# Kernel optimization log

Measured on AMD Instinct MI355X. Metric: run time of the kernel, lower is better.

Reference implementation:

```python
import jax, jax.numpy as jnp
import numpy as np

NNZ = 1_000_000
M = N = 8192
K = 128

def setup_inputs() -> dict:
    key = jax.random.key(0)
    k1, k2, k3, k4, k5 = jax.random.split(key, 5)
    mask_vals = jax.random.normal(k1, (NNZ,), dtype=jnp.float32)
    rows = jax.random.randint(k2, (NNZ,), 0, M, dtype=jnp.int64)
    cols = jax.random.randint(k3, (NNZ,), 0, N, dtype=jnp.int64)
    mat1 = jax.random.normal(k4, (M, K), dtype=jnp.float32)
    mat2 = jax.random.normal(k5, (K, N), dtype=jnp.float32)
    return {"mask_vals": mask_vals, "rows": rows, "cols": cols,
            "mat1": mat1, "mat2": mat2}

def reference(mask_vals, rows, cols, mat1, mat2):
    # torch.sparse.sampled_addmm with alpha=beta=1:
    # out.values = mask.values + (mat1 @ mat2)[rows, cols]
    # SDDMM: only compute the dot products at the sampled (row, col) pairs.
    a = mat1[rows]        # [nnz, K] gather of mat1 rows
    b = mat2[:, cols].T   # [nnz, K] gather of mat2 cols
    sampled = jnp.einsum('nk,nk->n', a, b)  # per-nnz dot product
    return mask_vals + sampled
```

## Files before the change

### kernel.cpp

```cpp
#include <hip/hip_runtime.h>
#include <hip/hip_fp16.h>


#define KDIM 128
#define NBUCK 64
#define SLAB_COLS 128
#define NBLK 512
#define SUBS 16

typedef _Float16 half2v __attribute__((ext_vector_type(2)));

union F4H8 {
  float4 f4;
  half2v h2[4];
  _Float16 h[8];
};


__global__ __launch_bounds__(256) void convert_f16_kernel(
    const float* __restrict__ in, _Float16* __restrict__ out, int n) {
  int i = (blockIdx.x * 256 + threadIdx.x) * 8;
  if (i >= n) return;
  const float4* p = (const float4*)(in + i);
  float4 x0 = p[0];
  float4 x1 = p[1];
  F4H8 o;
  o.h[0] = (_Float16)x0.x; o.h[1] = (_Float16)x0.y;
  o.h[2] = (_Float16)x0.z; o.h[3] = (_Float16)x0.w;
  o.h[4] = (_Float16)x1.x; o.h[5] = (_Float16)x1.y;
  o.h[6] = (_Float16)x1.z; o.h[7] = (_Float16)x1.w;
  *(float4*)(out + i) = o.f4;
}

__global__ __launch_bounds__(256) void transpose_f16_kernel(
    const float* __restrict__ in, _Float16* __restrict__ out, int N) {
  __shared__ float tile[32][33];
  int bx = blockIdx.x * 32;
  int by = blockIdx.y * 32;
  int tx = threadIdx.x;
  int ty = threadIdx.y;
#pragma unroll
  for (int j = 0; j < 32; j += 8) {
    tile[ty + j][tx] = in[(size_t)(by + ty + j) * N + (bx + tx)];
  }
  __syncthreads();
#pragma unroll
  for (int j = 0; j < 32; j += 8) {
    out[(size_t)(bx + ty + j) * KDIM + (by + tx)] = (_Float16)tile[tx][ty + j];
  }
}


__global__ __launch_bounds__(256) void hist_kernel(
    const int* __restrict__ cols, int nnz, int epb,
    int* __restrict__ blockHist) {
  __shared__ int h[NBUCK];
  if (threadIdx.x < NBUCK) h[threadIdx.x] = 0;
  __syncthreads();
  int lo = blockIdx.x * epb;
  int hi = min(lo + epb, nnz);
  for (int i = lo + threadIdx.x; i < hi; i += 256) {
    atomicAdd(&h[cols[i] >> 7], 1);
  }
  __syncthreads();
  if (threadIdx.x < NBUCK) {
    blockHist[blockIdx.x * NBUCK + threadIdx.x] = h[threadIdx.x];
  }
}

__global__ __launch_bounds__(NBLK) void colscan_kernel(
    const int* __restrict__ blockHist, int* __restrict__ blockScan,
    int* __restrict__ totals) {
  __shared__ int sh[NBLK];
  int b = blockIdx.x;
  int t = threadIdx.x;
  int v = blockHist[t * NBUCK + b];
  sh[t] = v;
  __syncthreads();
  for (int off = 1; off < NBLK; off <<= 1) {
    int x = (t >= off) ? sh[t - off] : 0;
    __syncthreads();
    sh[t] += x;
    __syncthreads();
  }
  blockScan[t * NBUCK + b] = sh[t] - v;
  if (t == NBLK - 1) totals[b] = sh[t];
}

__global__ __launch_bounds__(64) void base_kernel(
    const int* __restrict__ totals, int* __restrict__ bucketBase) {
  if (threadIdx.x == 0) {
    int acc = 0;
    for (int b = 0; b < NBUCK; ++b) {
      bucketBase[b] = acc;
      acc += totals[b];
      acc = (acc + 7) & ~7;
    }
    bucketBase[NBUCK] = acc;
  }
}

__global__ __launch_bounds__(256) void scatter_kernel(
    const int* __restrict__ rows, const int* __restrict__ cols,
    const float* __restrict__ mask, int nnz, int epb,
    const int* __restrict__ blockScan, const int* __restrict__ bucketBase,
    int* __restrict__ sortedRC, float* __restrict__ sortedMask,
    int* __restrict__ sortedIdx) {
  __shared__ int h[NBUCK];
  if (threadIdx.x < NBUCK) h[threadIdx.x] = 0;
  __syncthreads();
  int blk = blockIdx.x;
  int lo = blk * epb;
  int hi = min(lo + epb, nnz);
  for (int i = lo + threadIdx.x; i < hi; i += 256) {
    int c = cols[i];
    int r = rows[i];
    float mv = mask[i];
    int b = c >> 7;
    int rank = atomicAdd(&h[b], 1);
    int pos = bucketBase[b] + blockScan[blk * NBUCK + b] + rank;
    sortedRC[pos] = (r << 16) | c;
    sortedMask[pos] = mv;
    sortedIdx[pos] = i;
  }
}


__device__ __forceinline__ float dot8(const F4H8& a, const F4H8& b) {
  float s = 0.f;
#if __has_builtin(__builtin_amdgcn_fdot2)
#pragma unroll
  for (int j = 0; j < 4; ++j) s = __builtin_amdgcn_fdot2(a.h2[j], b.h2[j], s, false);
#else
#pragma unroll
  for (int j = 0; j < 8; ++j) s += (float)a.h[j] * (float)b.h[j];
#endif
  return s;
}

__device__ __forceinline__ float red16(float s) {
  s += __shfl_xor(s, 8);
  s += __shfl_xor(s, 4);
  s += __shfl_xor(s, 2);
  s += __shfl_xor(s, 1);
  return s;
}

__global__ __launch_bounds__(512) void sddmm_slab_kernel(
    const _Float16* __restrict__ m1,
    const _Float16* __restrict__ m2t,
    const int* __restrict__ sortedRC,
    const float* __restrict__ sortedMask,
    const int* __restrict__ sortedIdx,
    const int* __restrict__ bucketBase,
    const int* __restrict__ totals,
    float* __restrict__ out) {
  __shared__ _Float16 slab[SLAB_COLS * KDIM];
  int s = blockIdx.x / SUBS;
  int sub = blockIdx.x % SUBS;

  {
    const float4* src = (const float4*)(m2t + (size_t)s * SLAB_COLS * KDIM);
    float4* dst = (float4*)slab;
#pragma unroll
    for (int i = 0; i < (SLAB_COLS * KDIM / 8) / 512; ++i) {
      dst[threadIdx.x + i * 512] = src[threadIdx.x + i * 512];
    }
  }
  __syncthreads();

  int start = bucketBase[s];
  int cnt = totals[s];
  int hi0 = start + cnt;
  int per = ((cnt + SUBS - 1) / SUBS + 3) & ~3;
  int lo = start + sub * per;
  int hi = min(lo + per, hi0);

  int grp = threadIdx.x >> 4;
  int lane = threadIdx.x & 15;

  for (int g0 = lo + grp * 4; g0 < hi; g0 += 32 * 4) {
    if (g0 + 4 <= hi) {
      int4 rc4 = *(const int4*)(sortedRC + g0);
      float4 mv4 = *(const float4*)(sortedMask + g0);
      int4 idx4 = *(const int4*)(sortedIdx + g0);

      F4H8 a0, a1, a2, a3, b0, b1, b2, b3;
      a0.f4 = ((const float4*)(m1 + (size_t)(rc4.x >> 16) * KDIM))[lane];
      a1.f4 = ((const float4*)(m1 + (size_t)(rc4.y >> 16) * KDIM))[lane];
      a2.f4 = ((const float4*)(m1 + (size_t)(rc4.z >> 16) * KDIM))[lane];
      a3.f4 = ((const float4*)(m1 + (size_t)(rc4.w >> 16) * KDIM))[lane];
      b0.f4 = ((const float4*)(slab + (rc4.x & (SLAB_COLS - 1)) * KDIM))[lane];
      b1.f4 = ((const float4*)(slab + (rc4.y & (SLAB_COLS - 1)) * KDIM))[lane];
      b2.f4 = ((const float4*)(slab + (rc4.z & (SLAB_COLS - 1)) * KDIM))[lane];
      b3.f4 = ((const float4*)(slab + (rc4.w & (SLAB_COLS - 1)) * KDIM))[lane];

      float s0 = red16(dot8(a0, b0));
      float s1 = red16(dot8(a1, b1));
      float s2 = red16(dot8(a2, b2));
      float s3 = red16(dot8(a3, b3));

      if (lane == 0) {
        out[idx4.x] = mv4.x + s0;
        out[idx4.y] = mv4.y + s1;
        out[idx4.z] = mv4.z + s2;
        out[idx4.w] = mv4.w + s3;
      }
    } else {
      for (int g = g0; g < hi; ++g) {
        int rc = sortedRC[g];
        F4H8 a, b;
        a.f4 = ((const float4*)(m1 + (size_t)(rc >> 16) * KDIM))[lane];
        b.f4 = ((const float4*)(slab + (rc & (SLAB_COLS - 1)) * KDIM))[lane];
        float sv = red16(dot8(a, b));
        if (lane == 0) out[sortedIdx[g]] = sortedMask[g] + sv;
      }
    }
  }
}


__global__ __launch_bounds__(256) void sddmm_f16_b4_kernel(
    const float* __restrict__ mask_vals, const int* __restrict__ rows,
    const int* __restrict__ cols, const _Float16* __restrict__ m1,
    const _Float16* __restrict__ m2t, float* __restrict__ out, int nnz) {
  int tid = blockIdx.x * 256 + threadIdx.x;
  int grp = tid >> 4;
  int lane = tid & 15;
  int g0 = grp * 4;
  if (g0 >= nnz) return;
  if (g0 + 4 <= nnz) {
    int4 r4 = *(const int4*)(rows + g0);
    int4 c4 = *(const int4*)(cols + g0);
    F4H8 a0, a1, a2, a3, b0, b1, b2, b3;
    a0.f4 = ((const float4*)(m1 + (size_t)r4.x * KDIM))[lane];
    a1.f4 = ((const float4*)(m1 + (size_t)r4.y * KDIM))[lane];
    a2.f4 = ((const float4*)(m1 + (size_t)r4.z * KDIM))[lane];
    a3.f4 = ((const float4*)(m1 + (size_t)r4.w * KDIM))[lane];
    b0.f4 = ((const float4*)(m2t + (size_t)c4.x * KDIM))[lane];
    b1.f4 = ((const float4*)(m2t + (size_t)c4.y * KDIM))[lane];
    b2.f4 = ((const float4*)(m2t + (size_t)c4.z * KDIM))[lane];
    b3.f4 = ((const float4*)(m2t + (size_t)c4.w * KDIM))[lane];
    float s0 = red16(dot8(a0, b0));
    float s1 = red16(dot8(a1, b1));
    float s2 = red16(dot8(a2, b2));
    float s3 = red16(dot8(a3, b3));
    if (lane == 0) {
      float4 mv = *(const float4*)(mask_vals + g0);
      float4 o = {mv.x + s0, mv.y + s1, mv.z + s2, mv.w + s3};
      *(float4*)(out + g0) = o;
    }
  } else {
    for (int g = g0; g < nnz; ++g) {
      F4H8 a, b;
      a.f4 = ((const float4*)(m1 + (size_t)rows[g] * KDIM))[lane];
      b.f4 = ((const float4*)(m2t + (size_t)cols[g] * KDIM))[lane];
      float sv = red16(dot8(a, b));
      if (lane == 0) out[g] = mask_vals[g] + sv;
    }
  }
}

__global__ __launch_bounds__(256) void sddmm16_strided_kernel(
    const float* __restrict__ mask_vals, const int* __restrict__ rows,
    const int* __restrict__ cols, const float* __restrict__ mat1,
    const float* __restrict__ mat2, float* __restrict__ out, int nnz, int N) {
  int tid = blockIdx.x * 256 + threadIdx.x;
  int g = tid >> 4;
  int lane = tid & 15;
  if (g >= nnz) return;
  int r = rows[g];
  int c = cols[g];
  const float* arow = mat1 + (size_t)r * KDIM;
  float s = 0.f;
#pragma unroll
  for (int j = 0; j < 8; ++j) {
    int k = lane + 16 * j;
    s += arow[k] * mat2[(size_t)k * N + c];
  }
  s = red16(s);
  if (lane == 0) out[g] = mask_vals[g] + s;
}


extern "C" void kernel_launch(void* const* d_in, const int* in_sizes, int n_in,
                              void* d_out, int out_size, void* d_ws, size_t ws_size,
                              hipStream_t stream) {
  const float* mask_vals = (const float*)d_in[0];
  const int*   rows      = (const int*)d_in[1];
  const int*   cols      = (const int*)d_in[2];
  const float* mat1      = (const float*)d_in[3];
  const float* mat2      = (const float*)d_in[4];
  float*       out       = (float*)d_out;

  int nnz   = in_sizes[0];
  int m1_sz = in_sizes[3];
  int N     = in_sizes[4] / KDIM;

  auto align256 = [](size_t x) { return (x + 255) & ~(size_t)255; };
  size_t off = 0;
  size_t o_m1h   = off; off = align256(off + (size_t)m1_sz * 2);
  size_t o_m2th  = off; off = align256(off + (size_t)KDIM * N * 2);
  size_t cap     = (size_t)nnz + 8 * NBUCK + 64;
  size_t o_rc    = off; off = align256(off + cap * 4);
  size_t o_mk    = off; off = align256(off + cap * 4);
  size_t o_ix    = off; off = align256(off + cap * 4);
  size_t o_bh    = off; off = align256(off + (size_t)NBLK * NBUCK * 4);
  size_t o_bs    = off; off = align256(off + (size_t)NBLK * NBUCK * 4);
  size_t o_tot   = off; off = align256(off + NBUCK * 4);
  size_t o_base  = off; off = align256(off + (NBUCK + 1) * 4);
  size_t need_full = off;
  size_t need_min  = align256((size_t)m1_sz * 2) + align256((size_t)KDIM * N * 2);

  char* ws = (char*)d_ws;

  if (ws_size >= need_full && N == 8192) {
    _Float16* m1h   = (_Float16*)(ws + o_m1h);
    _Float16* m2th  = (_Float16*)(ws + o_m2th);
    int*      sRC   = (int*)(ws + o_rc);
    float*    sMK   = (float*)(ws + o_mk);
    int*      sIX   = (int*)(ws + o_ix);
    int*      bh    = (int*)(ws + o_bh);
    int*      bs    = (int*)(ws + o_bs);
    int*      tot   = (int*)(ws + o_tot);
    int*      bbase = (int*)(ws + o_base);

    convert_f16_kernel<<<(m1_sz / 8 + 255) / 256, 256, 0, stream>>>(mat1, m1h, m1_sz);
    dim3 tb(32, 8);
    dim3 tg(N / 32, KDIM / 32);
    transpose_f16_kernel<<<tg, tb, 0, stream>>>(mat2, m2th, N);

    int epb = (nnz + NBLK - 1) / NBLK;
    hist_kernel<<<NBLK, 256, 0, stream>>>(cols, nnz, epb, bh);
    colscan_kernel<<<NBUCK, NBLK, 0, stream>>>(bh, bs, tot);
    base_kernel<<<1, 64, 0, stream>>>(tot, bbase);
    scatter_kernel<<<NBLK, 256, 0, stream>>>(rows, cols, mask_vals, nnz, epb,
                                             bs, bbase, sRC, sMK, sIX);
    sddmm_slab_kernel<<<NBUCK * SUBS, 512, 0, stream>>>(m1h, m2th, sRC, sMK,
                                                        sIX, bbase, tot, out);
  } else if (ws_size >= need_min) {
    _Float16* m1h  = (_Float16*)ws;
    _Float16* m2th = m1h + m1_sz;
    convert_f16_kernel<<<(m1_sz / 8 + 255) / 256, 256, 0, stream>>>(mat1, m1h, m1_sz);
    dim3 tb(32, 8);
    dim3 tg(N / 32, KDIM / 32);
    transpose_f16_kernel<<<tg, tb, 0, stream>>>(mat2, m2th, N);
    int groups = (nnz + 3) / 4;
    int blocks = (groups * 16 + 255) / 256;
    sddmm_f16_b4_kernel<<<blocks, 256, 0, stream>>>(mask_vals, rows, cols, m1h,
                                                    m2th, out, nnz);
  } else {
    int blocks = ((size_t)nnz * 16 + 255) / 256;
    sddmm16_strided_kernel<<<blocks, 256, 0, stream>>>(mask_vals, rows, cols,
                                                       mat1, mat2, out, nnz, N);
  }
}
```

Baseline: 122.6 us.

## Fuse prep kernels, replace block scan with atomic cursors, pack sort records

Merges the fp16 conversion and the transpose into one launch. The per-block histogram and column scan are replaced by global atomic totals, a single-wave shuffle scan, and per-block atomic cursor reservation inside scatter, which now counts locally a second time. Row/col, index and mask are packed into one int4 record per element, so the SDDMM kernel issues one load per element instead of three separate arrays. This cuts the launch count and the scan overhead but makes the bucket ordering nondeterministic, re-reads cols in scatter, and writes 16 bytes per record instead of 12.

```diff
diff --git a/kernel.cpp b/kernel.cpp
--- a/kernel.cpp
+++ b/kernel.cpp
@@ -15,6 +15,208 @@
   half2v h2[4];
   _Float16 h[8];
 };
+
+
+__global__ __launch_bounds__(256) void prep_kernel(
+    const float* __restrict__ mat1, _Float16* __restrict__ m1h, int m1_sz,
+    const float* __restrict__ mat2, _Float16* __restrict__ m2th, int N,
+    int* __restrict__ tot, int nconvblk) {
+  __shared__ float tile[32][33];
+  int blk = blockIdx.x;
+  if (blk < nconvblk) {
+    if (blk == 0 && threadIdx.x < NBUCK) tot[threadIdx.x] = 0;
+    int i = (blk * 256 + threadIdx.x) * 8;
+    if (i < m1_sz) {
+      const float4* p = (const float4*)(mat1 + i);
+      float4 x0 = p[0];
+      float4 x1 = p[1];
+      F4H8 o;
+      o.h[0] = (_Float16)x0.x; o.h[1] = (_Float16)x0.y;
+      o.h[2] = (_Float16)x0.z; o.h[3] = (_Float16)x0.w;
+      o.h[4] = (_Float16)x1.x; o.h[5] = (_Float16)x1.y;
+      o.h[6] = (_Float16)x1.z; o.h[7] = (_Float16)x1.w;
+      *(float4*)(m1h + i) = o.f4;
+    }
+    return;
+  }
+  int u = blk - nconvblk;
+  int nbx = N / 32;
+  int bx = (u % nbx) * 32;
+  int by = (u / nbx) * 32;
+  int tx = threadIdx.x & 31;
+  int ty = threadIdx.x >> 5;
+#pragma unroll
+  for (int j = 0; j < 32; j += 8) {
+    tile[ty + j][tx] = mat2[(size_t)(by + ty + j) * N + (bx + tx)];
+  }
+  __syncthreads();
+#pragma unroll
+  for (int j = 0; j < 32; j += 8) {
+    m2th[(size_t)(bx + ty + j) * KDIM + (by + tx)] = (_Float16)tile[tx][ty + j];
+  }
+}
+
+
+__global__ __launch_bounds__(256) void hist_kernel(
+    const int* __restrict__ cols, int nnz, int epb, int* __restrict__ tot) {
+  __shared__ int h[NBUCK];
+  if (threadIdx.x < NBUCK) h[threadIdx.x] = 0;
+  __syncthreads();
+  int lo = blockIdx.x * epb;
+  int hi = min(lo + epb, nnz);
+  for (int i = lo + threadIdx.x; i < hi; i += 256) {
+    atomicAdd(&h[cols[i] >> 7], 1);
+  }
+  __syncthreads();
+  if (threadIdx.x < NBUCK && h[threadIdx.x]) {
+    atomicAdd(&tot[threadIdx.x], h[threadIdx.x]);
+  }
+}
+
+
+__global__ __launch_bounds__(64) void scan_kernel(
+    const int* __restrict__ tot, int* __restrict__ bbase,
+    int* __restrict__ cursor) {
+  int t = threadIdx.x;
+  int v = (tot[t] + 7) & ~7;
+  int inc = v;
+#pragma unroll
+  for (int off = 1; off < 64; off <<= 1) {
+    int x = __shfl_up(inc, off);
+    if (t >= off) inc += x;
+  }
+  int base = inc - v;
+  bbase[t] = base;
+  cursor[t] = base;
+}
+
+
+__global__ __launch_bounds__(256) void scatter_kernel(
+    const int* __restrict__ rows, const int* __restrict__ cols,
+    const float* __restrict__ mask, int nnz, int epb,
+    int* __restrict__ cursor, int4* __restrict__ recs) {
+  __shared__ int h[NBUCK];
+  __shared__ int startS[NBUCK];
+  if (threadIdx.x < NBUCK) h[threadIdx.x] = 0;
+  __syncthreads();
+  int lo = blockIdx.x * epb;
+  int hi = min(lo + epb, nnz);
+  for (int i = lo + threadIdx.x; i < hi; i += 256) {
+    atomicAdd(&h[cols[i] >> 7], 1);
+  }
+  __syncthreads();
+  if (threadIdx.x < NBUCK) {
+    int c = h[threadIdx.x];
+    startS[threadIdx.x] = c ? atomicAdd(&cursor[threadIdx.x], c) : 0;
+    h[threadIdx.x] = 0;
+  }
+  __syncthreads();
+  for (int i = lo + threadIdx.x; i < hi; i += 256) {
+    int c = cols[i];
+    int b = c >> 7;
+    int rank = atomicAdd(&h[b], 1);
+    int pos = startS[b] + rank;
+    int4 rec;
+    rec.x = (rows[i] << 16) | c;
+    rec.y = i;
+    rec.z = __float_as_int(mask[i]);
+    rec.w = 0;
+    recs[pos] = rec;
+  }
+}
+
+
+__device__ __forceinline__ float dot8(const F4H8& a, const F4H8& b) {
+  float s = 0.f;
+#if __has_builtin(__builtin_amdgcn_fdot2)
+#pragma unroll
+  for (int j = 0; j < 4; ++j) s = __builtin_amdgcn_fdot2(a.h2[j], b.h2[j], s, false);
+#else
+#pragma unroll
+  for (int j = 0; j < 8; ++j) s += (float)a.h[j] * (float)b.h[j];
+#endif
+  return s;
+}
+
+__device__ __forceinline__ float red16(float s) {
+  s += __shfl_xor(s, 8);
+  s += __shfl_xor(s, 4);
+  s += __shfl_xor(s, 2);
+  s += __shfl_xor(s, 1);
+  return s;
+}
+
+__global__ __launch_bounds__(512) void sddmm_slab_kernel(
+    const _Float16* __restrict__ m1,
+    const _Float16* __restrict__ m2t,
+    const int4* __restrict__ recs,
+    const int* __restrict__ bbase,
+    const int* __restrict__ tot,
+    float* __restrict__ out) {
+  __shared__ _Float16 slab[SLAB_COLS * KDIM];
+  int s = blockIdx.x / SUBS;
+  int sub = blockIdx.x % SUBS;
+
+  {
+    const float4* src = (const float4*)(m2t + (size_t)s * SLAB_COLS * KDIM);
+    float4* dst = (float4*)slab;
+#pragma unroll
+    for (int i = 0; i < 4; ++i) {
+      dst[threadIdx.x + i * 512] = src[threadIdx.x + i * 512];
+    }
+  }
+  __syncthreads();
+
+  int start = bbase[s];
+  int cnt = tot[s];
+  int hi0 = start + cnt;
+  int per = ((cnt + SUBS - 1) / SUBS + 3) & ~3;
+  int lo = start + sub * per;
+  int hi = min(lo + per, hi0);
+
+  int grp = threadIdx.x >> 4;
+  int lane = threadIdx.x & 15;
+
+  for (int g0 = lo + grp * 4; g0 < hi; g0 += 32 * 4) {
+    if (g0 + 4 <= hi) {
+      int4 r0 = recs[g0];
+      int4 r1 = recs[g0 + 1];
+      int4 r2 = recs[g0 + 2];
+      int4 r3 = recs[g0 + 3];
+
+      F4H8 a0, a1, a2, a3, b0, b1, b2, b3;
+      a0.f4 = ((const float4*)(m1 + (size_t)((unsigned)r0.x >> 16) * KDIM))[lane];
+      a1.f4 = ((const float4*)(m1 + (size_t)((unsigned)r1.x >> 16) * KDIM))[lane];
+      a2.f4 = ((const float4*)(m1 + (size_t)((unsigned)r2.x >> 16) * KDIM))[lane];
+      a3.f4 = ((const float4*)(m1 + (size_t)((unsigned)r3.x >> 16) * KDIM))[lane];
+      b0.f4 = ((const float4*)(slab + (r0.x & (SLAB_COLS - 1)) * KDIM))[lane];
+      b1.f4 = ((const float4*)(slab + (r1.x & (SLAB_COLS - 1)) * KDIM))[lane];
+      b2.f4 = ((const float4*)(slab + (r2.x & (SLAB_COLS - 1)) * KDIM))[lane];
+      b3.f4 = ((const float4*)(slab + (r3.x & (SLAB_COLS - 1)) * KDIM))[lane];
+
+      float s0 = red16(dot8(a0, b0));
+      float s1 = red16(dot8(a1, b1));
+      float s2 = red16(dot8(a2, b2));
+      float s3 = red16(dot8(a3, b3));
+
+      if (lane == 0) {
+        out[r0.y] = __int_as_float(r0.z) + s0;
+        out[r1.y] = __int_as_float(r1.z) + s1;
+        out[r2.y] = __int_as_float(r2.z) + s2;
+        out[r3.y] = __int_as_float(r3.z) + s3;
+      }
+    } else {
+      for (int g = g0; g < hi; ++g) {
+        int4 r = recs[g];
+        F4H8 a, b;
+        a.f4 = ((const float4*)(m1 + (size_t)((unsigned)r.x >> 16) * KDIM))[lane];
+        b.f4 = ((const float4*)(slab + (r.x & (SLAB_COLS - 1)) * KDIM))[lane];
+        float sv = red16(dot8(a, b));
+        if (lane == 0) out[r.y] = __int_as_float(r.z) + sv;
+      }
+    }
+  }
+}
 
 
 __global__ __launch_bounds__(256) void convert_f16_kernel(
@@ -49,176 +251,6 @@
     out[(size_t)(bx + ty + j) * KDIM + (by + tx)] = (_Float16)tile[tx][ty + j];
   }
 }
-
-
-__global__ __launch_bounds__(256) void hist_kernel(
-    const int* __restrict__ cols, int nnz, int epb,
-    int* __restrict__ blockHist) {
-  __shared__ int h[NBUCK];
-  if (threadIdx.x < NBUCK) h[threadIdx.x] = 0;
-  __syncthreads();
-  int lo = blockIdx.x * epb;
-  int hi = min(lo + epb, nnz);
-  for (int i = lo + threadIdx.x; i < hi; i += 256) {
-    atomicAdd(&h[cols[i] >> 7], 1);
-  }
-  __syncthreads();
-  if (threadIdx.x < NBUCK) {
-    blockHist[blockIdx.x * NBUCK + threadIdx.x] = h[threadIdx.x];
-  }
-}
-
-__global__ __launch_bounds__(NBLK) void colscan_kernel(
-    const int* __restrict__ blockHist, int* __restrict__ blockScan,
-    int* __restrict__ totals) {
-  __shared__ int sh[NBLK];
-  int b = blockIdx.x;
-  int t = threadIdx.x;
-  int v = blockHist[t * NBUCK + b];
-  sh[t] = v;
-  __syncthreads();
-  for (int off = 1; off < NBLK; off <<= 1) {
-    int x = (t >= off) ? sh[t - off] : 0;
-    __syncthreads();
-    sh[t] += x;
-    __syncthreads();
-  }
-  blockScan[t * NBUCK + b] = sh[t] - v;
-  if (t == NBLK - 1) totals[b] = sh[t];
-}
-
-__global__ __launch_bounds__(64) void base_kernel(
-    const int* __restrict__ totals, int* __restrict__ bucketBase) {
-  if (threadIdx.x == 0) {
-    int acc = 0;
-    for (int b = 0; b < NBUCK; ++b) {
-      bucketBase[b] = acc;
-      acc += totals[b];
-      acc = (acc + 7) & ~7;
-    }
-    bucketBase[NBUCK] = acc;
-  }
-}
-
-__global__ __launch_bounds__(256) void scatter_kernel(
-    const int* __restrict__ rows, const int* __restrict__ cols,
-    const float* __restrict__ mask, int nnz, int epb,
-    const int* __restrict__ blockScan, const int* __restrict__ bucketBase,
-    int* __restrict__ sortedRC, float* __restrict__ sortedMask,
-    int* __restrict__ sortedIdx) {
-  __shared__ int h[NBUCK];
-  if (threadIdx.x < NBUCK) h[threadIdx.x] = 0;
-  __syncthreads();
-  int blk = blockIdx.x;
-  int lo = blk * epb;
-  int hi = min(lo + epb, nnz);
-  for (int i = lo + threadIdx.x; i < hi; i += 256) {
-    int c = cols[i];
-    int r = rows[i];
-    float mv = mask[i];
-    int b = c >> 7;
-    int rank = atomicAdd(&h[b], 1);
-    int pos = bucketBase[b] + blockScan[blk * NBUCK + b] + rank;
-    sortedRC[pos] = (r << 16) | c;
-    sortedMask[pos] = mv;
-    sortedIdx[pos] = i;
-  }
-}
-
-
-__device__ __forceinline__ float dot8(const F4H8& a, const F4H8& b) {
-  float s = 0.f;
-#if __has_builtin(__builtin_amdgcn_fdot2)
-#pragma unroll
-  for (int j = 0; j < 4; ++j) s = __builtin_amdgcn_fdot2(a.h2[j], b.h2[j], s, false);
-#else
-#pragma unroll
-  for (int j = 0; j < 8; ++j) s += (float)a.h[j] * (float)b.h[j];
-#endif
-  return s;
-}
-
-__device__ __forceinline__ float red16(float s) {
-  s += __shfl_xor(s, 8);
-  s += __shfl_xor(s, 4);
-  s += __shfl_xor(s, 2);
-  s += __shfl_xor(s, 1);
-  return s;
-}
-
-__global__ __launch_bounds__(512) void sddmm_slab_kernel(
-    const _Float16* __restrict__ m1,
-    const _Float16* __restrict__ m2t,
-    const int* __restrict__ sortedRC,
-    const float* __restrict__ sortedMask,
-    const int* __restrict__ sortedIdx,
-    const int* __restrict__ bucketBase,
-    const int* __restrict__ totals,
-    float* __restrict__ out) {
-  __shared__ _Float16 slab[SLAB_COLS * KDIM];
-  int s = blockIdx.x / SUBS;
-  int sub = blockIdx.x % SUBS;
-
-  {
-    const float4* src = (const float4*)(m2t + (size_t)s * SLAB_COLS * KDIM);
-    float4* dst = (float4*)slab;
-#pragma unroll
-    for (int i = 0; i < (SLAB_COLS * KDIM / 8) / 512; ++i) {
-      dst[threadIdx.x + i * 512] = src[threadIdx.x + i * 512];
-    }
-  }
-  __syncthreads();
-
-  int start = bucketBase[s];
-  int cnt = totals[s];
-  int hi0 = start + cnt;
-  int per = ((cnt + SUBS - 1) / SUBS + 3) & ~3;
-  int lo = start + sub * per;
-  int hi = min(lo + per, hi0);
-
-  int grp = threadIdx.x >> 4;
-  int lane = threadIdx.x & 15;
-
-  for (int g0 = lo + grp * 4; g0 < hi; g0 += 32 * 4) {
-    if (g0 + 4 <= hi) {
-      int4 rc4 = *(const int4*)(sortedRC + g0);
-      float4 mv4 = *(const float4*)(sortedMask + g0);
-      int4 idx4 = *(const int4*)(sortedIdx + g0);
-
-      F4H8 a0, a1, a2, a3, b0, b1, b2, b3;
-      a0.f4 = ((const float4*)(m1 + (size_t)(rc4.x >> 16) * KDIM))[lane];
-      a1.f4 = ((const float4*)(m1 + (size_t)(rc4.y >> 16) * KDIM))[lane];
-      a2.f4 = ((const float4*)(m1 + (size_t)(rc4.z >> 16) * KDIM))[lane];
-      a3.f4 = ((const float4*)(m1 + (size_t)(rc4.w >> 16) * KDIM))[lane];
-      b0.f4 = ((const float4*)(slab + (rc4.x & (SLAB_COLS - 1)) * KDIM))[lane];
-      b1.f4 = ((const float4*)(slab + (rc4.y & (SLAB_COLS - 1)) * KDIM))[lane];
-      b2.f4 = ((const float4*)(slab + (rc4.z & (SLAB_COLS - 1)) * KDIM))[lane];
-      b3.f4 = ((const float4*)(slab + (rc4.w & (SLAB_COLS - 1)) * KDIM))[lane];
-
-      float s0 = red16(dot8(a0, b0));
-      float s1 = red16(dot8(a1, b1));
-      float s2 = red16(dot8(a2, b2));
-      float s3 = red16(dot8(a3, b3));
-
-      if (lane == 0) {
-        out[idx4.x] = mv4.x + s0;
-        out[idx4.y] = mv4.y + s1;
-        out[idx4.z] = mv4.z + s2;
-        out[idx4.w] = mv4.w + s3;
-      }
-    } else {
-      for (int g = g0; g < hi; ++g) {
-        int rc = sortedRC[g];
-        F4H8 a, b;
-        a.f4 = ((const float4*)(m1 + (size_t)(rc >> 16) * KDIM))[lane];
-        b.f4 = ((const float4*)(slab + (rc & (SLAB_COLS - 1)) * KDIM))[lane];
-        float sv = red16(dot8(a, b));
-        if (lane == 0) out[sortedIdx[g]] = sortedMask[g] + sv;
-      }
-    }
-  }
-}
-
 
 __global__ __launch_bounds__(256) void sddmm_f16_b4_kernel(
     const float* __restrict__ mask_vals, const int* __restrict__ rows,
@@ -299,45 +331,38 @@
 
   auto align256 = [](size_t x) { return (x + 255) & ~(size_t)255; };
   size_t off = 0;
-  size_t o_m1h   = off; off = align256(off + (size_t)m1_sz * 2);
-  size_t o_m2th  = off; off = align256(off + (size_t)KDIM * N * 2);
-  size_t cap     = (size_t)nnz + 8 * NBUCK + 64;
-  size_t o_rc    = off; off = align256(off + cap * 4);
-  size_t o_mk    = off; off = align256(off + cap * 4);
-  size_t o_ix    = off; off = align256(off + cap * 4);
-  size_t o_bh    = off; off = align256(off + (size_t)NBLK * NBUCK * 4);
-  size_t o_bs    = off; off = align256(off + (size_t)NBLK * NBUCK * 4);
-  size_t o_tot   = off; off = align256(off + NBUCK * 4);
-  size_t o_base  = off; off = align256(off + (NBUCK + 1) * 4);
+  size_t o_m1h  = off; off = align256(off + (size_t)m1_sz * 2);
+  size_t o_m2th = off; off = align256(off + (size_t)KDIM * N * 2);
+  size_t cap    = (size_t)nnz + 8 * NBUCK + 64;
+  size_t o_rec  = off; off = align256(off + cap * 16);
+  size_t o_tot  = off; off = align256(off + NBUCK * 4);
+  size_t o_bb   = off; off = align256(off + NBUCK * 4);
+  size_t o_cur  = off; off = align256(off + NBUCK * 4);
   size_t need_full = off;
   size_t need_min  = align256((size_t)m1_sz * 2) + align256((size_t)KDIM * N * 2);
 
   char* ws = (char*)d_ws;
 
-  if (ws_size >= need_full && N == 8192) {
-    _Float16* m1h   = (_Float16*)(ws + o_m1h);
-    _Float16* m2th  = (_Float16*)(ws + o_m2th);
-    int*      sRC   = (int*)(ws + o_rc);
-    float*    sMK   = (float*)(ws + o_mk);
-    int*      sIX   = (int*)(ws + o_ix);
-    int*      bh    = (int*)(ws + o_bh);
-    int*      bs    = (int*)(ws + o_bs);
-    int*      tot   = (int*)(ws + o_tot);
-    int*      bbase = (int*)(ws + o_base);
-
-    convert_f16_kernel<<<(m1_sz / 8 + 255) / 256, 256, 0, stream>>>(mat1, m1h, m1_sz);
-    dim3 tb(32, 8);
-    dim3 tg(N / 32, KDIM / 32);
-    transpose_f16_kernel<<<tg, tb, 0, stream>>>(mat2, m2th, N);
+  if (ws_size >= need_full && N == NBUCK * SLAB_COLS && m1_sz % 2048 == 0) {
+    _Float16* m1h  = (_Float16*)(ws + o_m1h);
+    _Float16* m2th = (_Float16*)(ws + o_m2th);
+    int4*     recs = (int4*)(ws + o_rec);
+    int*      tot  = (int*)(ws + o_tot);
+    int*      bb   = (int*)(ws + o_bb);
+    int*      cur  = (int*)(ws + o_cur);
+
+    int nconvblk  = (m1_sz / 8 + 255) / 256;
+    int ntransblk = (N / 32) * (KDIM / 32);
+    prep_kernel<<<nconvblk + ntransblk, 256, 0, stream>>>(
+        mat1, m1h, m1_sz, mat2, m2th, N, tot, nconvblk);
 
     int epb = (nnz + NBLK - 1) / NBLK;
-    hist_kernel<<<NBLK, 256, 0, stream>>>(cols, nnz, epb, bh);
-    colscan_kernel<<<NBUCK, NBLK, 0, stream>>>(bh, bs, tot);
-    base_kernel<<<1, 64, 0, stream>>>(tot, bbase);
+    hist_kernel<<<NBLK, 256, 0, stream>>>(cols, nnz, epb, tot);
+    scan_kernel<<<1, 64, 0, stream>>>(tot, bb, cur);
     scatter_kernel<<<NBLK, 256, 0, stream>>>(rows, cols, mask_vals, nnz, epb,
-                                             bs, bbase, sRC, sMK, sIX);
-    sddmm_slab_kernel<<<NBUCK * SUBS, 512, 0, stream>>>(m1h, m2th, sRC, sMK,
-                                                        sIX, bbase, tot, out);
+                                             cur, recs);
+    sddmm_slab_kernel<<<NBUCK * SUBS, 512, 0, stream>>>(m1h, m2th, recs, bb,
+                                                        tot, out);
   } else if (ws_size >= need_min) {
     _Float16* m1h  = (_Float16*)ws;
     _Float16* m2th = m1h + m1_sz;
```

Measured after the change: 132.3 us. 7.9% more time.
